# Performance work log

Hardware: AMD Instinct MI355X
Metric: run time of the kernel (lower is better)

The kernel has to match this reference:

```python
import jax, jax.numpy as jnp
import numpy as np

NUM_LEVELS = 16
BASE_RES = 16
MAX_RES = 2048
TABLE_SIZE = 1 << 19
FEATS = 2
GROWTH = np.exp((np.log(MAX_RES) - np.log(BASE_RES)) / (NUM_LEVELS - 1))
SCALINGS = jnp.asarray(np.floor(BASE_RES * GROWTH ** np.arange(NUM_LEVELS)), dtype=jnp.float32)  # [L]
OFFSETS = jnp.arange(NUM_LEVELS, dtype=jnp.int32) * TABLE_SIZE  # per-level slice offset into table
AABB_MIN, AABB_MAX = -1.0, 1.0
P1, P2 = jnp.uint32(2654435761), jnp.uint32(805459861)
MASK = jnp.uint32(TABLE_SIZE - 1)


def sh16(d):
    # spherical harmonics components, levels=4 -> 16 components (nerfstudio convention)
    x, y, z = d[..., 0], d[..., 1], d[..., 2]
    xx, yy, zz = x * x, y * y, z * z
    return jnp.stack([
        jnp.full_like(x, 0.28209479177387814),
        -0.48860251190291987 * y,
        0.48860251190291987 * z,
        -0.48860251190291987 * x,
        1.0925484305920792 * x * y,
        -1.0925484305920792 * y * z,
        0.94617469575755997 * zz - 0.31539156525251999,
        -1.0925484305920792 * x * z,
        0.54627421529603959 * (xx - yy),
        0.59004358992664352 * y * (3.0 * xx - yy),
        2.8906114426405538 * x * y * z,
        0.45704579946446572 * y * (5.0 * zz - 1.0),
        0.37317633259011546 * z * (5.0 * zz - 3.0),
        0.45704579946446572 * x * (5.0 * zz - 1.0),
        1.4453057213202769 * z * (xx - yy),
        0.59004358992664352 * x * (xx - 3.0 * yy),
    ], axis=-1)


def hash_fn(x, y, z):
    # spatial hash with wraparound uint32 arithmetic; lower 19 bits match int64 math mod 2^19
    v = x ^ (y * P1) ^ (z * P2)
    return (v & MASK).astype(jnp.int32) + OFFSETS  # [N, L]


def hash_encode(pts, table):
    # pts: [N,3] in [0,1]; table: [L*T, F]
    scaled = pts[:, None, :] * SCALINGS[None, :, None]  # [N, L, 3]
    f = jnp.floor(scaled)
    c = jnp.ceil(scaled)
    off = scaled - f  # [N, L, 3]
    fi = f.astype(jnp.uint32)
    ci = c.astype(jnp.uint32)
    cx, cy, cz = ci[..., 0], ci[..., 1], ci[..., 2]
    fx, fy, fz = fi[..., 0], fi[..., 1], fi[..., 2]
    # corner order matches nerfstudio hashed_0..7
    idx = jnp.stack([
        hash_fn(cx, cy, cz), hash_fn(cx, fy, cz), hash_fn(fx, fy, cz), hash_fn(fx, cy, cz),
        hash_fn(cx, cy, fz), hash_fn(cx, fy, fz), hash_fn(fx, fy, fz), hash_fn(fx, cy, fz),
    ], axis=0)  # [8, N, L]
    feats = table[idx]  # [8, N, L, F]
    ox, oy, oz = off[..., 0:1], off[..., 1:2], off[..., 2:3]
    f03 = feats[0] * ox + feats[3] * (1.0 - ox)
    f12 = feats[1] * ox + feats[2] * (1.0 - ox)
    f56 = feats[5] * ox + feats[6] * (1.0 - ox)
    f47 = feats[4] * ox + feats[7] * (1.0 - ox)
    f0312 = f03 * oy + f12 * (1.0 - oy)
    f4756 = f47 * oy + f56 * (1.0 - oy)
    enc = f0312 * oz + f4756 * (1.0 - oz)  # [N, L, F]
    return enc.reshape(enc.shape[0], NUM_LEVELS * FEATS)


def setup_inputs() -> dict:
    key = jax.random.key(0)
    ks = jax.random.split(key, 16)
    B, S = 4096, 48
    positions = jax.random.uniform(ks[0], (B, S, 3), jnp.float32) * 2.0 - 1.0
    densities = jax.random.normal(ks[1], (B, S, 1), jnp.float32)
    normals = jax.random.normal(ks[2], (B, 3), jnp.float32)
    camera_to_worlds = jax.random.normal(ks[3], (B, 3, 4), jnp.float32) * 0.3
    hash_table = (jax.random.uniform(ks[4], (NUM_LEVELS * TABLE_SIZE, FEATS), jnp.float32) * 2.0 - 1.0) * 1e-4
    def lin(k, i, o):
        return jax.random.normal(k, (i, o), jnp.float32) * (1.0 / np.sqrt(i))
    return {
        'positions': positions, 'densities': densities, 'normals': normals,
        'camera_to_worlds': camera_to_worlds, 'hash_table': hash_table,
        'w1': lin(ks[5], 32, 64), 'b1': jnp.zeros((64,), jnp.float32),
        'w2': lin(ks[6], 64, 16), 'b2': jnp.zeros((16,), jnp.float32),
        'h1': lin(ks[7], 32, 64), 'hb1': jnp.zeros((64,), jnp.float32),
        'h2': lin(ks[8], 64, 64), 'hb2': jnp.zeros((64,), jnp.float32),
        'h3': lin(ks[9], 64, 3), 'hb3': jnp.zeros((3,), jnp.float32),
    }


def reference(positions, densities, normals, camera_to_worlds, hash_table,
              w1, b1, w2, b2, h1, hb1, h2, hb2, h3, hb3):
    B, S, _ = positions.shape
    R = camera_to_worlds[..., :3, :3]
    t = camera_to_worlds[..., :3, 3]
    Rinv = jnp.swapaxes(R, -1, -2)  # pose inverse for rigid transform
    tinv = -jnp.einsum('bij,bj->bi', Rinv, t)
    pos = jnp.einsum('bij,bsj->bsi', Rinv, positions) + tinv[:, None, :]  # world -> camera
    pos = (pos - AABB_MIN) / (AABB_MAX - AABB_MIN)  # SceneBox.get_normalized_positions
    n_cam = jnp.einsum('bij,bj->bi', Rinv, normals)
    n_cam = (n_cam + 1.0) / 2.0  # get_normalized_directions
    d = sh16(n_cam)  # [B, 16]
    d = jnp.broadcast_to(d[:, None, :], (B, S, 16)).reshape(-1, 16)
    selector = jnp.all((pos > 0.0) & (pos < 1.0), axis=-1)
    pos = pos * selector[..., None]
    enc = hash_encode(pos.reshape(-1, 3), hash_table)  # [B*S, 32]
    geo = jax.nn.relu(jax.nn.relu(enc @ w1 + b1) @ w2 + b2)  # mlp_base, out ReLU
    h = jnp.concatenate([d, geo], axis=-1)  # [B*S, 32]
    rgb = jax.nn.sigmoid(jax.nn.relu(jax.nn.relu(h @ h1 + hb1) @ h2 + hb2) @ h3 + hb3)
    rgb = rgb.reshape(B, S, 3)
    weight = jax.nn.softmax(densities, axis=-2)  # softmax over samples
    return jnp.sum(weight * rgb, axis=-2)  # [B, 3] == FieldHeadNames.RGB_AFFINE
```

## Files before the change

kernel.cpp:

```cpp
#include <hip/hip_runtime.h>
#include <math.h>
#include <stdint.h>

#define NLEV 16
#define TSIZE (1u << 19)
#define NB 4096
#define NS 48
#define NPTS (NB * NS)

typedef __attribute__((ext_vector_type(8))) short short8;
typedef __attribute__((ext_vector_type(4))) float f32x4;

struct Scales { float s[NLEV]; };

__device__ __forceinline__ uint32_t hash3(uint32_t x, uint32_t y, uint32_t z) {
    return (x ^ (y * 2654435761u) ^ (z * 805459861u)) & (TSIZE - 1u);
}

__device__ __forceinline__ float sigmoidf(float v) {
    return 1.0f / (1.0f + expf(-v));
}

__device__ __forceinline__ ushort f2b(float f) {
    union { float f; uint32_t u; } v; v.f = f;
    uint32_t r = (v.u + 0x7FFFu + ((v.u >> 16) & 1u)) >> 16;
    return (ushort)r;
}

#define LDS_FENCE() asm volatile("s_waitcnt lgkmcnt(0)" ::: "memory")

#define MFMA16(a, b, c) __builtin_amdgcn_mfma_f32_16x16x32_bf16((a), (b), (c), 0, 0, 0)

__global__ __launch_bounds__(256) void encode_kernel(
    const float* __restrict__ positions,
    const float* __restrict__ c2w,
    const float* __restrict__ table,
    const float* __restrict__ w1, const float* __restrict__ w2,
    const float* __restrict__ h1, const float* __restrict__ h2,
    const float* __restrict__ h3,
    uint32_t* __restrict__ enc_ws,
    ushort* __restrict__ bank,
    Scales sc)
{
    const int bid = blockIdx.x;
    if (bid == (NPTS / 256) * NLEV) {
        for (int idx = threadIdx.x; idx < 20 * 512; idx += 256) {
            const int f    = idx >> 9;
            const int r    = idx & 511;
            const int lane = r >> 3;
            const int j    = r & 7;
            const int l15  = lane & 15;
            const int quad = lane >> 4;
            const int k8   = quad * 8 + j;
            float val;
            if (f < 4) {
                val = w1[k8 * 64 + f * 16 + l15];
            } else if (f < 6) {
                val = w2[((f - 4) * 32 + k8) * 16 + l15];
            } else if (f < 10) {
                val = h1[k8 * 64 + (f - 6) * 16 + l15];
            } else if (f < 18) {
                const int t = f - 10, nt = t >> 1, kk = t & 1;
                val = h2[(kk * 32 + k8) * 64 + nt * 16 + l15];
            } else {
                val = (l15 < 3) ? h3[((f - 18) * 32 + k8) * 3 + l15] : 0.0f;
            }
            bank[idx] = f2b(val);
        }
        return;
    }

    const int l = bid & 15;
    const int p = (bid >> 4) * 256 + threadIdx.x;
    const int b = p / NS;

    const float* M = c2w + b * 12;
    const float px = positions[3 * p + 0];
    const float py = positions[3 * p + 1];
    const float pz = positions[3 * p + 2];
    const float dx = px - M[3], dy = py - M[7], dz = pz - M[11];
    float qx = M[0] * dx + M[4] * dy + M[8] * dz;
    float qy = M[1] * dx + M[5] * dy + M[9] * dz;
    float qz = M[2] * dx + M[6] * dy + M[10] * dz;
    qx = (qx + 1.0f) * 0.5f;
    qy = (qy + 1.0f) * 0.5f;
    qz = (qz + 1.0f) * 0.5f;
    const bool sel = (qx > 0.0f) && (qx < 1.0f) &&
                     (qy > 0.0f) && (qy < 1.0f) &&
                     (qz > 0.0f) && (qz < 1.0f);
    if (!sel) { qx = 0.0f; qy = 0.0f; qz = 0.0f; }

    const float s = sc.s[l];
    const float sx = qx * s, sy = qy * s, sz = qz * s;
    const float fx = floorf(sx), fy = floorf(sy), fz = floorf(sz);
    const float cx = ceilf(sx),  cy = ceilf(sy),  cz = ceilf(sz);
    const float ox = sx - fx, oy = sy - fy, oz = sz - fz;
    const uint32_t fxi = (uint32_t)fx, fyi = (uint32_t)fy, fzi = (uint32_t)fz;
    const uint32_t cxi = (uint32_t)cx, cyi = (uint32_t)cy, czi = (uint32_t)cz;

    const float2* tab = (const float2*)table + (uint32_t)l * TSIZE;
    const float2 g0 = tab[hash3(cxi, cyi, czi)];
    const float2 g1 = tab[hash3(cxi, fyi, czi)];
    const float2 g2 = tab[hash3(fxi, fyi, czi)];
    const float2 g3 = tab[hash3(fxi, cyi, czi)];
    const float2 g4 = tab[hash3(cxi, cyi, fzi)];
    const float2 g5 = tab[hash3(cxi, fyi, fzi)];
    const float2 g6 = tab[hash3(fxi, fyi, fzi)];
    const float2 g7 = tab[hash3(fxi, cyi, fzi)];

    const float omx = 1.0f - ox, omy = 1.0f - oy, omz = 1.0f - oz;
    float f03x = g0.x * ox + g3.x * omx, f03y = g0.y * ox + g3.y * omx;
    float f12x = g1.x * ox + g2.x * omx, f12y = g1.y * ox + g2.y * omx;
    float f56x = g5.x * ox + g6.x * omx, f56y = g5.y * ox + g6.y * omx;
    float f47x = g4.x * ox + g7.x * omx, f47y = g4.y * ox + g7.y * omx;
    float ax = f03x * oy + f12x * omy, ay = f03y * oy + f12y * omy;
    float bx = f47x * oy + f56x * omy, by = f47y * oy + f56y * omy;
    const float ex = ax * oz + bx * omz;
    const float ey = ay * oz + by * omz;
    enc_ws[l * NPTS + p] = ((uint32_t)f2b(ey) << 16) | (uint32_t)f2b(ex);
}

__global__ __launch_bounds__(64) void tail_kernel(
    const uint32_t* __restrict__ enc_ws,
    const float* __restrict__ densities,
    const float* __restrict__ normals,
    const float* __restrict__ c2w,
    const ushort* __restrict__ bank,
    const float* __restrict__ b1, const float* __restrict__ b2,
    const float* __restrict__ hb1, const float* __restrict__ hb2,
    const float* __restrict__ hb3,
    float* __restrict__ out)
{
    __shared__ ushort bufA[48 * 72];
    __shared__ ushort bufB[48 * 72];
    __shared__ ushort bufC[48 * 40];

    const int bidb = blockIdx.x;
    const int p0   = bidb * NS;
    const int lane = threadIdx.x;
    const int l15  = lane & 15;
    const int quad = lane >> 4;

#pragma unroll
    for (int i = 0; i < 12; ++i) {
        const int flat = i * 64 + lane;
        const int l = flat / 48;
        const int j = flat - l * 48;
        *(uint32_t*)&bufA[j * 72 + 2 * l] = enc_ws[l * NPTS + p0 + j];
    }

    {
        const float* M = c2w + bidb * 12;
        const float n0 = normals[3 * bidb + 0];
        const float n1 = normals[3 * bidb + 1];
        const float n2 = normals[3 * bidb + 2];
        float x = M[0] * n0 + M[4] * n1 + M[8] * n2;
        float y = M[1] * n0 + M[5] * n1 + M[9] * n2;
        float z = M[2] * n0 + M[6] * n1 + M[10] * n2;
        x = (x + 1.0f) * 0.5f;
        y = (y + 1.0f) * 0.5f;
        z = (z + 1.0f) * 0.5f;
        const float xx = x * x, yy = y * y, zz = z * z;
        float v = 0.28209479177387814f;
        v = (l15 == 1)  ? -0.48860251190291987f * y : v;
        v = (l15 == 2)  ?  0.48860251190291987f * z : v;
        v = (l15 == 3)  ? -0.48860251190291987f * x : v;
        v = (l15 == 4)  ?  1.0925484305920792f * x * y : v;
        v = (l15 == 5)  ? -1.0925484305920792f * y * z : v;
        v = (l15 == 6)  ?  0.94617469575756f * zz - 0.31539156525252f : v;
        v = (l15 == 7)  ? -1.0925484305920792f * x * z : v;
        v = (l15 == 8)  ?  0.5462742152960396f * (xx - yy) : v;
        v = (l15 == 9)  ?  0.5900435899266435f * y * (3.0f * xx - yy) : v;
        v = (l15 == 10) ?  2.890611442640554f * x * y * z : v;
        v = (l15 == 11) ?  0.4570457994644657f * y * (5.0f * zz - 1.0f) : v;
        v = (l15 == 12) ?  0.37317633259011546f * z * (5.0f * zz - 3.0f) : v;
        v = (l15 == 13) ?  0.4570457994644657f * x * (5.0f * zz - 1.0f) : v;
        v = (l15 == 14) ?  1.445305721320277f * z * (xx - yy) : v;
        v = (l15 == 15) ?  0.5900435899266435f * x * (xx - 3.0f * yy) : v;
        const ushort shb = f2b(v);
#pragma unroll
        for (int i = 0; i < 12; ++i) {
            bufC[(i * 4 + quad) * 40 + l15] = shb;
        }
    }

    float b1v[4], hb1v[4], hb2v[4];
#pragma unroll
    for (int nt = 0; nt < 4; ++nt) {
        b1v[nt]  = b1[nt * 16 + l15];
        hb1v[nt] = hb1[nt * 16 + l15];
        hb2v[nt] = hb2[nt * 16 + l15];
    }
    const float b2v  = b2[l15];
    const float hb3v = (l15 < 3) ? hb3[l15] : 0.0f;

    const ushort* fb = bank + lane * 8;
#define FRAG(f) (*(const short8*)(fb + (f) * 512))

    const f32x4 zero = {0.0f, 0.0f, 0.0f, 0.0f};
    LDS_FENCE();

    {
        short8 w[4];
#pragma unroll
        for (int nt = 0; nt < 4; ++nt) w[nt] = FRAG(nt);
        f32x4 c[3][4];
#pragma unroll
        for (int t = 0; t < 3; ++t) {
            const short8 a = *(const short8*)&bufA[(16 * t + l15) * 72 + quad * 8];
#pragma unroll
            for (int nt = 0; nt < 4; ++nt) c[t][nt] = MFMA16(a, w[nt], zero);
        }
        LDS_FENCE();
#pragma unroll
        for (int t = 0; t < 3; ++t)
#pragma unroll
            for (int nt = 0; nt < 4; ++nt)
#pragma unroll
                for (int r = 0; r < 4; ++r) {
                    const float v = fmaxf(c[t][nt][r] + b1v[nt], 0.0f);
                    bufB[(16 * t + quad * 4 + r) * 72 + nt * 16 + l15] = f2b(v);
                }
    }
    LDS_FENCE();

    {
        const short8 w0 = FRAG(4), w1f = FRAG(5);
#pragma unroll
        for (int t = 0; t < 3; ++t) {
            const short8 a0 = *(const short8*)&bufB[(16 * t + l15) * 72 + quad * 8];
            const short8 a1 = *(const short8*)&bufB[(16 * t + l15) * 72 + 32 + quad * 8];
            f32x4 c = MFMA16(a0, w0, zero);
            c = MFMA16(a1, w1f, c);
#pragma unroll
            for (int r = 0; r < 4; ++r) {
                const float v = fmaxf(c[r] + b2v, 0.0f);
                bufC[(16 * t + quad * 4 + r) * 40 + 16 + l15] = f2b(v);
            }
        }
    }
    LDS_FENCE();

    {
        short8 w[4];
#pragma unroll
        for (int nt = 0; nt < 4; ++nt) w[nt] = FRAG(6 + nt);
        f32x4 c[3][4];
#pragma unroll
        for (int t = 0; t < 3; ++t) {
            const short8 a = *(const short8*)&bufC[(16 * t + l15) * 40 + quad * 8];
#pragma unroll
            for (int nt = 0; nt < 4; ++nt) c[t][nt] = MFMA16(a, w[nt], zero);
        }
        LDS_FENCE();
#pragma unroll
        for (int t = 0; t < 3; ++t)
#pragma unroll
            for (int nt = 0; nt < 4; ++nt)
#pragma unroll
                for (int r = 0; r < 4; ++r) {
                    const float v = fmaxf(c[t][nt][r] + hb1v[nt], 0.0f);
                    bufA[(16 * t + quad * 4 + r) * 72 + nt * 16 + l15] = f2b(v);
                }
    }
    LDS_FENCE();

    {
        short8 w[8];
#pragma unroll
        for (int f = 0; f < 8; ++f) w[f] = FRAG(10 + f);
        f32x4 c[3][4];
#pragma unroll
        for (int t = 0; t < 3; ++t) {
            const short8 a0 = *(const short8*)&bufA[(16 * t + l15) * 72 + quad * 8];
            const short8 a1 = *(const short8*)&bufA[(16 * t + l15) * 72 + 32 + quad * 8];
#pragma unroll
            for (int nt = 0; nt < 4; ++nt) {
                f32x4 u = MFMA16(a0, w[nt * 2], zero);
                c[t][nt] = MFMA16(a1, w[nt * 2 + 1], u);
            }
        }
        LDS_FENCE();
#pragma unroll
        for (int t = 0; t < 3; ++t)
#pragma unroll
            for (int nt = 0; nt < 4; ++nt)
#pragma unroll
                for (int r = 0; r < 4; ++r) {
                    const float v = fmaxf(c[t][nt][r] + hb2v[nt], 0.0f);
                    bufB[(16 * t + quad * 4 + r) * 72 + nt * 16 + l15] = f2b(v);
                }
    }
    LDS_FENCE();

    f32x4 rgbc[3];
    {
        const short8 w0 = FRAG(18), w1f = FRAG(19);
#pragma unroll
        for (int t = 0; t < 3; ++t) {
            const short8 a0 = *(const short8*)&bufB[(16 * t + l15) * 72 + quad * 8];
            const short8 a1 = *(const short8*)&bufB[(16 * t + l15) * 72 + 32 + quad * 8];
            f32x4 c = MFMA16(a0, w0, zero);
            rgbc[t] = MFMA16(a1, w1f, c);
        }
    }
#undef FRAG

    const float d = (lane < NS) ? densities[p0 + lane] : -INFINITY;
    float m = d;
#pragma unroll
    for (int off = 32; off > 0; off >>= 1) m = fmaxf(m, __shfl_xor(m, off));
    const float e = expf(d - m);
    float sum = e;
#pragma unroll
    for (int off = 32; off > 0; off >>= 1) sum += __shfl_xor(sum, off);
    const float wgt = e / sum;

    float* sW = (float*)bufC;
    LDS_FENCE();
    if (lane < NS) sW[lane] = wgt;
    LDS_FENCE();

    float acc = 0.0f;
#pragma unroll
    for (int t = 0; t < 3; ++t)
#pragma unroll
        for (int r = 0; r < 4; ++r) {
            const int row = 16 * t + quad * 4 + r;
            acc += sW[row] * sigmoidf(rgbc[t][r] + hb3v);
        }
    acc += __shfl_xor(acc, 16);
    acc += __shfl_xor(acc, 32);
    if (lane < 3) out[bidb * 3 + lane] = acc;
}

extern "C" void kernel_launch(void* const* d_in, const int* in_sizes, int n_in,
                              void* d_out, int out_size, void* d_ws, size_t ws_size,
                              hipStream_t stream) {
    const float* positions = (const float*)d_in[0];
    const float* densities = (const float*)d_in[1];
    const float* normals   = (const float*)d_in[2];
    const float* c2w       = (const float*)d_in[3];
    const float* table     = (const float*)d_in[4];
    const float* w1  = (const float*)d_in[5];
    const float* b1  = (const float*)d_in[6];
    const float* w2  = (const float*)d_in[7];
    const float* b2  = (const float*)d_in[8];
    const float* h1  = (const float*)d_in[9];
    const float* hb1 = (const float*)d_in[10];
    const float* h2  = (const float*)d_in[11];
    const float* hb2 = (const float*)d_in[12];
    const float* h3  = (const float*)d_in[13];
    const float* hb3 = (const float*)d_in[14];
    float* out = (float*)d_out;

    ushort*   bank   = (ushort*)d_ws;
    uint32_t* enc_ws = (uint32_t*)((char*)d_ws + 20 * 1024);

    Scales sc;
    const double growth = exp((log(2048.0) - log(16.0)) / 15.0);
    for (int i = 0; i < NLEV; ++i)
        sc.s[i] = (float)floor(16.0 * pow(growth, (double)i));

    const int enc_blocks = (NPTS / 256) * NLEV + 1;
    encode_kernel<<<enc_blocks, 256, 0, stream>>>(
        positions, c2w, table, w1, w2, h1, h2, h3, enc_ws, bank, sc);
    tail_kernel<<<NB, 64, 0, stream>>>(
        enc_ws, densities, normals, c2w, bank, b1, b2, hb1, hb2, hb3, out);
}
```

Before: 217.8 us.

## Transpose tail MFMAs, load encodings into registers, and reorder encode level scheduling

Swaps the MFMA operand order in the tail kernel so each lane owns contiguous output columns. This lets activations be packed and written to LDS as 64-bit stores, and lets the first layer's encoded inputs load straight from global memory into registers without an LDS staging pass. The final weighted sigmoid reduction now uses shuffles instead of an LDS round trip, and MFMA sections are wrapped in s_setprio. The encode kernel reorders block-to-level mapping into two phases that interleave coarse and fine levels, likely to balance cache pressure on the hash table. Several LDS fences are removed, which depends on the new data flow being correct.

```diff
diff --git a/kernel.cpp b/kernel.cpp
--- a/kernel.cpp
+++ b/kernel.cpp
@@ -7,6 +7,7 @@
 #define NB 4096
 #define NS 48
 #define NPTS (NB * NS)
+#define CHUNKS (NPTS / 256)
 
 typedef __attribute__((ext_vector_type(8))) short short8;
 typedef __attribute__((ext_vector_type(4))) float f32x4;
@@ -25,6 +26,19 @@
     union { float f; uint32_t u; } v; v.f = f;
     uint32_t r = (v.u + 0x7FFFu + ((v.u >> 16) & 1u)) >> 16;
     return (ushort)r;
+}
+
+__device__ __forceinline__ uint32_t pk_relu2(float a, float b) {
+    a = fmaxf(a, 0.0f);
+    b = fmaxf(b, 0.0f);
+    return ((uint32_t)f2b(b) << 16) | (uint32_t)f2b(a);
+}
+
+__device__ __forceinline__ uint2 pack4_relu(f32x4 c, f32x4 bias) {
+    uint2 o;
+    o.x = pk_relu2(c[0] + bias[0], c[1] + bias[1]);
+    o.y = pk_relu2(c[2] + bias[2], c[3] + bias[3]);
+    return o;
 }
 
 #define LDS_FENCE() asm volatile("s_waitcnt lgkmcnt(0)" ::: "memory")
@@ -43,7 +57,7 @@
     Scales sc)
 {
     const int bid = blockIdx.x;
-    if (bid == (NPTS / 256) * NLEV) {
+    if (bid == CHUNKS * NLEV) {
         for (int idx = threadIdx.x; idx < 20 * 512; idx += 256) {
             const int f    = idx >> 9;
             const int r    = idx & 511;
@@ -70,9 +84,13 @@
         return;
     }
 
-    const int l = bid & 15;
-    const int p = (bid >> 4) * 256 + threadIdx.x;
-    const int b = p / NS;
+    const int half  = CHUNKS * 8;
+    const int ph    = (bid >= half) ? 1 : 0;
+    const int q     = bid - ph * half;
+    const int x     = q & 7;
+    const int l     = x + 8 * ((x & 1) ^ ph);
+    const int p     = (q >> 3) * 256 + threadIdx.x;
+    const int b     = p / NS;
 
     const float* M = c2w + b * 12;
     const float px = positions[3 * p + 0];
@@ -141,13 +159,13 @@
     const int l15  = lane & 15;
     const int quad = lane >> 4;
 
-#pragma unroll
-    for (int i = 0; i < 12; ++i) {
-        const int flat = i * 64 + lane;
-        const int l = flat / 48;
-        const int j = flat - l * 48;
-        *(uint32_t*)&bufA[j * 72 + 2 * l] = enc_ws[l * NPTS + p0 + j];
-    }
+    union XU { uint32_t u[4]; short8 s; };
+    XU xu[3];
+#pragma unroll
+    for (int t = 0; t < 3; ++t)
+#pragma unroll
+        for (int jj = 0; jj < 4; ++jj)
+            xu[t].u[jj] = enc_ws[(quad * 4 + jj) * NPTS + p0 + 16 * t + l15];
 
     {
         const float* M = c2w + bidb * 12;
@@ -179,65 +197,54 @@
         v = (l15 == 15) ?  0.5900435899266435f * x * (xx - 3.0f * yy) : v;
         const ushort shb = f2b(v);
 #pragma unroll
-        for (int i = 0; i < 12; ++i) {
+        for (int i = 0; i < 12; ++i)
             bufC[(i * 4 + quad) * 40 + l15] = shb;
-        }
-    }
-
-    float b1v[4], hb1v[4], hb2v[4];
-#pragma unroll
-    for (int nt = 0; nt < 4; ++nt) {
-        b1v[nt]  = b1[nt * 16 + l15];
-        hb1v[nt] = hb1[nt * 16 + l15];
-        hb2v[nt] = hb2[nt * 16 + l15];
-    }
-    const float b2v  = b2[l15];
-    const float hb3v = (l15 < 3) ? hb3[l15] : 0.0f;
+    }
 
     const ushort* fb = bank + lane * 8;
 #define FRAG(f) (*(const short8*)(fb + (f) * 512))
 
     const f32x4 zero = {0.0f, 0.0f, 0.0f, 0.0f};
-    LDS_FENCE();
 
     {
         short8 w[4];
 #pragma unroll
         for (int nt = 0; nt < 4; ++nt) w[nt] = FRAG(nt);
         f32x4 c[3][4];
-#pragma unroll
-        for (int t = 0; t < 3; ++t) {
-            const short8 a = *(const short8*)&bufA[(16 * t + l15) * 72 + quad * 8];
-#pragma unroll
-            for (int nt = 0; nt < 4; ++nt) c[t][nt] = MFMA16(a, w[nt], zero);
-        }
-        LDS_FENCE();
+        __builtin_amdgcn_s_setprio(1);
+#pragma unroll
+        for (int t = 0; t < 3; ++t)
+#pragma unroll
+            for (int nt = 0; nt < 4; ++nt) c[t][nt] = MFMA16(w[nt], xu[t].s, zero);
+        __builtin_amdgcn_s_setprio(0);
+        f32x4 b1q[4];
+#pragma unroll
+        for (int nt = 0; nt < 4; ++nt) b1q[nt] = *(const f32x4*)&b1[nt * 16 + quad * 4];
 #pragma unroll
         for (int t = 0; t < 3; ++t)
 #pragma unroll
             for (int nt = 0; nt < 4; ++nt)
-#pragma unroll
-                for (int r = 0; r < 4; ++r) {
-                    const float v = fmaxf(c[t][nt][r] + b1v[nt], 0.0f);
-                    bufB[(16 * t + quad * 4 + r) * 72 + nt * 16 + l15] = f2b(v);
-                }
+                *(uint2*)&bufB[(16 * t + l15) * 72 + nt * 16 + quad * 4] =
+                    pack4_relu(c[t][nt], b1q[nt]);
     }
     LDS_FENCE();
 
     {
         const short8 w0 = FRAG(4), w1f = FRAG(5);
+        const f32x4 b2q = *(const f32x4*)&b2[quad * 4];
+        f32x4 c[3];
+        __builtin_amdgcn_s_setprio(1);
 #pragma unroll
         for (int t = 0; t < 3; ++t) {
             const short8 a0 = *(const short8*)&bufB[(16 * t + l15) * 72 + quad * 8];
             const short8 a1 = *(const short8*)&bufB[(16 * t + l15) * 72 + 32 + quad * 8];
-            f32x4 c = MFMA16(a0, w0, zero);
-            c = MFMA16(a1, w1f, c);
-#pragma unroll
-            for (int r = 0; r < 4; ++r) {
-                const float v = fmaxf(c[r] + b2v, 0.0f);
-                bufC[(16 * t + quad * 4 + r) * 40 + 16 + l15] = f2b(v);
-            }
-        }
+            c[t] = MFMA16(w0, a0, zero);
+            c[t] = MFMA16(w1f, a1, c[t]);
+        }
+        __builtin_amdgcn_s_setprio(0);
+#pragma unroll
+        for (int t = 0; t < 3; ++t)
+            *(uint2*)&bufC[(16 * t + l15) * 40 + 16 + quad * 4] = pack4_relu(c[t], b2q);
     }
     LDS_FENCE();
 
@@ -246,22 +253,23 @@
 #pragma unroll
         for (int nt = 0; nt < 4; ++nt) w[nt] = FRAG(6 + nt);
         f32x4 c[3][4];
+        __builtin_amdgcn_s_setprio(1);
 #pragma unroll
         for (int t = 0; t < 3; ++t) {
             const short8 a = *(const short8*)&bufC[(16 * t + l15) * 40 + quad * 8];
 #pragma unroll
-            for (int nt = 0; nt < 4; ++nt) c[t][nt] = MFMA16(a, w[nt], zero);
-        }
-        LDS_FENCE();
+            for (int nt = 0; nt < 4; ++nt) c[t][nt] = MFMA16(w[nt], a, zero);
+        }
+        __builtin_amdgcn_s_setprio(0);
+        f32x4 hb1q[4];
+#pragma unroll
+        for (int nt = 0; nt < 4; ++nt) hb1q[nt] = *(const f32x4*)&hb1[nt * 16 + quad * 4];
 #pragma unroll
         for (int t = 0; t < 3; ++t)
 #pragma unroll
             for (int nt = 0; nt < 4; ++nt)
-#pragma unroll
-                for (int r = 0; r < 4; ++r) {
-                    const float v = fmaxf(c[t][nt][r] + hb1v[nt], 0.0f);
-                    bufA[(16 * t + quad * 4 + r) * 72 + nt * 16 + l15] = f2b(v);
-                }
+                *(uint2*)&bufA[(16 * t + l15) * 72 + nt * 16 + quad * 4] =
+                    pack4_relu(c[t][nt], hb1q[nt]);
     }
     LDS_FENCE();
 
@@ -270,39 +278,42 @@
 #pragma unroll
         for (int f = 0; f < 8; ++f) w[f] = FRAG(10 + f);
         f32x4 c[3][4];
+        __builtin_amdgcn_s_setprio(1);
 #pragma unroll
         for (int t = 0; t < 3; ++t) {
             const short8 a0 = *(const short8*)&bufA[(16 * t + l15) * 72 + quad * 8];
             const short8 a1 = *(const short8*)&bufA[(16 * t + l15) * 72 + 32 + quad * 8];
 #pragma unroll
             for (int nt = 0; nt < 4; ++nt) {
-                f32x4 u = MFMA16(a0, w[nt * 2], zero);
-                c[t][nt] = MFMA16(a1, w[nt * 2 + 1], u);
+                f32x4 u = MFMA16(w[nt * 2], a0, zero);
+                c[t][nt] = MFMA16(w[nt * 2 + 1], a1, u);
             }
         }
-        LDS_FENCE();
+        __builtin_amdgcn_s_setprio(0);
+        f32x4 hb2q[4];
+#pragma unroll
+        for (int nt = 0; nt < 4; ++nt) hb2q[nt] = *(const f32x4*)&hb2[nt * 16 + quad * 4];
 #pragma unroll
         for (int t = 0; t < 3; ++t)
 #pragma unroll
             for (int nt = 0; nt < 4; ++nt)
-#pragma unroll
-                for (int r = 0; r < 4; ++r) {
-                    const float v = fmaxf(c[t][nt][r] + hb2v[nt], 0.0f);
-                    bufB[(16 * t + quad * 4 + r) * 72 + nt * 16 + l15] = f2b(v);
-                }
+                *(uint2*)&bufB[(16 * t + l15) * 72 + nt * 16 + quad * 4] =
+                    pack4_relu(c[t][nt], hb2q[nt]);
     }
     LDS_FENCE();
 
-    f32x4 rgbc[3];
+    f32x4 c5[3];
     {
         const short8 w0 = FRAG(18), w1f = FRAG(19);
+        __builtin_amdgcn_s_setprio(1);
 #pragma unroll
         for (int t = 0; t < 3; ++t) {
             const short8 a0 = *(const short8*)&bufB[(16 * t + l15) * 72 + quad * 8];
             const short8 a1 = *(const short8*)&bufB[(16 * t + l15) * 72 + 32 + quad * 8];
-            f32x4 c = MFMA16(a0, w0, zero);
-            rgbc[t] = MFMA16(a1, w1f, c);
-        }
+            c5[t] = MFMA16(w0, a0, zero);
+            c5[t] = MFMA16(w1f, a1, c5[t]);
+        }
+        __builtin_amdgcn_s_setprio(0);
     }
 #undef FRAG
 
@@ -315,23 +326,29 @@
 #pragma unroll
     for (int off = 32; off > 0; off >>= 1) sum += __shfl_xor(sum, off);
     const float wgt = e / sum;
-
-    float* sW = (float*)bufC;
-    LDS_FENCE();
-    if (lane < NS) sW[lane] = wgt;
-    LDS_FENCE();
-
-    float acc = 0.0f;
-#pragma unroll
-    for (int t = 0; t < 3; ++t)
-#pragma unroll
-        for (int r = 0; r < 4; ++r) {
-            const int row = 16 * t + quad * 4 + r;
-            acc += sW[row] * sigmoidf(rgbc[t][r] + hb3v);
-        }
-    acc += __shfl_xor(acc, 16);
-    acc += __shfl_xor(acc, 32);
-    if (lane < 3) out[bidb * 3 + lane] = acc;
+    float wt[3];
+#pragma unroll
+    for (int t = 0; t < 3; ++t) wt[t] = __shfl(wgt, 16 * t + l15);
+
+    const float h30 = hb3[0], h31 = hb3[1], h32 = hb3[2];
+    float a0 = 0.0f, a1 = 0.0f, a2 = 0.0f;
+#pragma unroll
+    for (int t = 0; t < 3; ++t) {
+        a0 += wt[t] * sigmoidf(c5[t][0] + h30);
+        a1 += wt[t] * sigmoidf(c5[t][1] + h31);
+        a2 += wt[t] * sigmoidf(c5[t][2] + h32);
+    }
+#pragma unroll
+    for (int off = 1; off < 16; off <<= 1) {
+        a0 += __shfl_xor(a0, off);
+        a1 += __shfl_xor(a1, off);
+        a2 += __shfl_xor(a2, off);
+    }
+    if (lane == 0) {
+        out[bidb * 3 + 0] = a0;
+        out[bidb * 3 + 1] = a1;
+        out[bidb * 3 + 2] = a2;
+    }
 }
 
 extern "C" void kernel_launch(void* const* d_in, const int* in_sizes, int n_in,
@@ -362,7 +379,7 @@
     for (int i = 0; i < NLEV; ++i)
         sc.s[i] = (float)floor(16.0 * pow(growth, (double)i));
 
-    const int enc_blocks = (NPTS / 256) * NLEV + 1;
+    const int enc_blocks = CHUNKS * NLEV + 1;
     encode_kernel<<<enc_blocks, 256, 0, stream>>>(
         positions, c2w, table, w1, w2, h1, h2, h3, enc_ws, bank, sc);
     tail_kernel<<<NB, 64, 0, stream>>>(
```

Result: faster. 203.2 us (-6.7%).
